# Kernel optimization log

Measured on AMD Instinct MI355X. Metric: run time of the kernel, lower is better.

The kernel has to match this reference:

```python
import jax, jax.numpy as jnp
import numpy as np

N, S, I, L, M = 4096, 8, 256, 512, 256


def setup_inputs() -> dict:
    key = jax.random.key(0)
    ks = jax.random.split(key, 13)
    sc_in = 1.0 / np.sqrt(I + L)
    sc_out = 1.0 / np.sqrt(L)
    return {
        "modulation": jax.random.normal(ks[0], (N, S * I), jnp.float32),
        "h0": jax.random.normal(ks[1], (N, S * L), jnp.float32),
        "c0": jax.random.normal(ks[2], (N, S * L), jnp.float32),
        "Wi": jax.random.normal(ks[3], (S, L, I + L), jnp.float32) * sc_in,
        "bi": jnp.full((S, L), -1.0, jnp.float32),  # init_input bias
        "Wf": jax.random.normal(ks[4], (S, L, I + L), jnp.float32) * sc_in,
        "bf": jnp.full((S, L), 1.0, jnp.float32),   # init_forget bias
        "Wg": jax.random.normal(ks[5], (S, L, I + L), jnp.float32) * sc_in,
        "bg": jnp.zeros((S, L), jnp.float32),
        "Wo": jax.random.normal(ks[6], (S, L, I + L), jnp.float32) * sc_in,
        "bo": jnp.zeros((S, L), jnp.float32),
        "Wy": jax.random.normal(ks[7], (S, M, L), jnp.float32) * sc_out,
        "by": jnp.zeros((S, M), jnp.float32),
    }


def reference(modulation, h0, c0, Wi, bi, Wf, bf, Wg, bg, Wo, bo, Wy, by):
    n = modulation.shape[0]
    x = modulation.reshape(n, S, I)          # [N,S,I]
    h = h0.reshape(n, S, L)                  # [N,S,L]
    c = c0.reshape(n, S, L)
    xh = jnp.concatenate([x, h], axis=-1)    # cat_groups: per-stream [x_s, h_s] -> [N,S,I+L]
    # grouped per-stream linear projections for the four gates
    i = jax.nn.sigmoid(jnp.einsum('nsd,sld->nsl', xh, Wi) + bi)
    f = jax.nn.sigmoid(jnp.einsum('nsd,sld->nsl', xh, Wf) + bf)
    g = jnp.tanh(jnp.einsum('nsd,sld->nsl', xh, Wg) + bg)
    o = jax.nn.sigmoid(jnp.einsum('nsd,sld->nsl', xh, Wo) + bo)
    c_new = f * c + i * g
    h_new = o * jnp.tanh(c_new)              # dropout p=0 -> identity
    y = jnp.einsum('nsl,sml->nsm', h_new, Wy) + by
    return y.reshape(n, S * M)
```

## Files before the change

### kernel.cpp

```cpp
#include <hip/hip_runtime.h>
#include <stdint.h>

#define S_ 8
#define N_ 4096
#define I_ 256
#define L_ 512
#define M_ 256
#define D_ 768

typedef __bf16 bf16x8 __attribute__((ext_vector_type(8)));
typedef float f32x4 __attribute__((ext_vector_type(4)));
typedef unsigned short ushort_t;

__device__ __forceinline__ unsigned short f2bf(float f) {
  union { float f; uint32_t u; } c; c.f = f;
  uint32_t u = c.u;
  uint32_t r = u + 0x7FFFu + ((u >> 16) & 1u);
  return (unsigned short)(r >> 16);
}

__device__ __forceinline__ float fsigmoid(float x) {
  return 1.0f / (1.0f + __expf(-x));
}
__device__ __forceinline__ float ftanh(float x) {
  float ax = fabsf(x);
  float e = __expf(-2.0f * ax);
  float t = (1.0f - e) / (1.0f + e);
  return copysignf(t, x);
}

#define GLD16(gsrc, ldst)                                                                  \
  __builtin_amdgcn_global_load_lds(                                                        \
      (const __attribute__((address_space(1))) uint32_t*)(uintptr_t)(gsrc),                \
      (__attribute__((address_space(3))) uint32_t*)(uintptr_t)(ldst), 16, 0, 0)


__global__ __launch_bounds__(256) void cast_bf16_kernel(const float* __restrict__ src,
                                                        ushort_t* __restrict__ dst, int n4) {
  int t = blockIdx.x * 256 + threadIdx.x;
  int stride = gridDim.x * 256;
  for (; t < n4; t += stride) {
    float4 v = ((const float4*)src)[t];
    ushort4 o;
    o.x = f2bf(v.x); o.y = f2bf(v.y); o.z = f2bf(v.z); o.w = f2bf(v.w);
    ((ushort4*)dst)[t] = o;
  }
}

__global__ __launch_bounds__(256) void build_xh_kernel(const float* __restrict__ mod,
                                                       const float* __restrict__ h0,
                                                       ushort_t* __restrict__ xh) {
  int t = blockIdx.x * 256 + threadIdx.x;
  const int total = S_ * N_ * (D_ / 4);
  int stride = gridDim.x * 256;
  for (; t < total; t += stride) {
    int row = t / (D_ / 4);
    int c = t - row * (D_ / 4);
    int s = row >> 12;
    int n = row & (N_ - 1);
    float4 v;
    if (c < I_ / 4)
      v = *(const float4*)(mod + (size_t)n * (S_ * I_) + s * I_ + c * 4);
    else
      v = *(const float4*)(h0 + (size_t)n * (S_ * L_) + s * L_ + (c - I_ / 4) * 4);
    ushort4 o;
    o.x = f2bf(v.x); o.y = f2bf(v.y); o.z = f2bf(v.z); o.w = f2bf(v.w);
    *(ushort4*)(xh + (size_t)t * 4) = o;
  }
}

__global__ __launch_bounds__(256, 2) void gates_kernel(
    const ushort_t* __restrict__ xh,
    const ushort_t* __restrict__ w4,
    const float* __restrict__ bi, const float* __restrict__ bff,
    const float* __restrict__ bg, const float* __restrict__ bo,
    const float* __restrict__ c0,
    ushort_t* __restrict__ hout)
{
  __shared__ __align__(16) ushort_t smem[3072 * 8];
  const int tid = threadIdx.x;
  const int lane = tid & 63;
  const int w = tid >> 6;
  const int n0 = blockIdx.x * 128;
  const int l0 = blockIdx.y * 64;
  const int s = blockIdx.z;

  f32x4 acc[4][2][4];
  #pragma unroll
  for (int g = 0; g < 4; ++g)
    #pragma unroll
    for (int rt = 0; rt < 2; ++rt)
      #pragma unroll
      for (int ct = 0; ct < 4; ++ct) {
        f32x4 z = {0.f, 0.f, 0.f, 0.f};
        acc[g][rt][ct] = z;
      }

  const size_t xh_row0 = (size_t)(s * N_ + n0) * D_;

  for (int t = 0; t < D_ / 64; ++t) {
    const int k0 = t * 64;
    #pragma unroll
    for (int it = 0; it < 4; ++it) {
      int chunk = it * 256 + tid;
      int r = chunk >> 3, c = chunk & 7;
      int cg = c ^ (r & 7);
      const ushort_t* src = xh + xh_row0 + (size_t)r * D_ + k0 + cg * 8;
      GLD16(src, &smem[(it * 256 + w * 64) * 8]);
    }
    #pragma unroll
    for (int it = 0; it < 8; ++it) {
      int chunk = it * 256 + tid;
      int g = chunk >> 9;
      int rl = (chunk >> 3) & 63;
      int c = chunk & 7;
      int cg = c ^ (rl & 7);
      const ushort_t* src = w4 + ((size_t)((g * S_ + s) * L_ + l0 + rl)) * D_ + k0 + cg * 8;
      GLD16(src, &smem[(1024 + it * 256 + w * 64) * 8]);
    }
    __syncthreads();
    #pragma unroll
    for (int kk = 0; kk < 2; ++kk) {
      const int cc = kk * 4 + (lane >> 4);
      bf16x8 a[2];
      #pragma unroll
      for (int rt = 0; rt < 2; ++rt) {
        int r = w * 32 + rt * 16 + (lane & 15);
        a[rt] = *(const bf16x8*)&smem[(r * 8 + (cc ^ (r & 7))) * 8];
      }
      #pragma unroll
      for (int g = 0; g < 4; ++g) {
        #pragma unroll
        for (int ct = 0; ct < 4; ++ct) {
          int rl = ct * 16 + (lane & 15);
          bf16x8 b = *(const bf16x8*)&smem[(1024 + (g * 64 + rl) * 8 + (cc ^ (rl & 7))) * 8];
          acc[g][0][ct] = __builtin_amdgcn_mfma_f32_16x16x32_bf16(a[0], b, acc[g][0][ct], 0, 0, 0);
          acc[g][1][ct] = __builtin_amdgcn_mfma_f32_16x16x32_bf16(a[1], b, acc[g][1][ct], 0, 0, 0);
        }
      }
    }
    __syncthreads();
  }

  #pragma unroll
  for (int ct = 0; ct < 4; ++ct) {
    const int l = l0 + ct * 16 + (lane & 15);
    const float vbi = bi[s * L_ + l];
    const float vbf = bff[s * L_ + l];
    const float vbg = bg[s * L_ + l];
    const float vbo = bo[s * L_ + l];
    #pragma unroll
    for (int rt = 0; rt < 2; ++rt) {
      #pragma unroll
      for (int j = 0; j < 4; ++j) {
        const int n = n0 + w * 32 + rt * 16 + (lane >> 4) * 4 + j;
        const float c0v = c0[(size_t)n * (S_ * L_) + s * L_ + l];
        const float iv = fsigmoid(acc[0][rt][ct][j] + vbi);
        const float fv = fsigmoid(acc[1][rt][ct][j] + vbf);
        const float gv = ftanh(acc[2][rt][ct][j] + vbg);
        const float ov = fsigmoid(acc[3][rt][ct][j] + vbo);
        const float cn = fv * c0v + iv * gv;
        const float hn = ov * ftanh(cn);
        hout[(size_t)(s * N_ + n) * L_ + l] = f2bf(hn);
      }
    }
  }
}

__global__ __launch_bounds__(256, 2) void out_kernel(
    const ushort_t* __restrict__ h,
    const ushort_t* __restrict__ wy,
    const float* __restrict__ by,
    float* __restrict__ out)
{
  __shared__ __align__(16) ushort_t smem[1536 * 8];
  const int tid = threadIdx.x;
  const int lane = tid & 63;
  const int w = tid >> 6;
  const int n0 = blockIdx.x * 128;
  const int m0 = blockIdx.y * 64;
  const int s = blockIdx.z;

  f32x4 acc[2][4];
  #pragma unroll
  for (int rt = 0; rt < 2; ++rt)
    #pragma unroll
    for (int ct = 0; ct < 4; ++ct) {
      f32x4 z = {0.f, 0.f, 0.f, 0.f};
      acc[rt][ct] = z;
    }

  const size_t h_row0 = (size_t)(s * N_ + n0) * L_;

  for (int t = 0; t < L_ / 64; ++t) {
    const int k0 = t * 64;
    #pragma unroll
    for (int it = 0; it < 4; ++it) {
      int chunk = it * 256 + tid;
      int r = chunk >> 3, c = chunk & 7;
      int cg = c ^ (r & 7);
      const ushort_t* src = h + h_row0 + (size_t)r * L_ + k0 + cg * 8;
      GLD16(src, &smem[(it * 256 + w * 64) * 8]);
    }
    #pragma unroll
    for (int it = 0; it < 2; ++it) {
      int chunk = it * 256 + tid;
      int rl = chunk >> 3, c = chunk & 7;
      int cg = c ^ (rl & 7);
      const ushort_t* src = wy + ((size_t)(s * M_ + m0 + rl)) * L_ + k0 + cg * 8;
      GLD16(src, &smem[(1024 + it * 256 + w * 64) * 8]);
    }
    __syncthreads();
    #pragma unroll
    for (int kk = 0; kk < 2; ++kk) {
      const int cc = kk * 4 + (lane >> 4);
      bf16x8 a[2];
      #pragma unroll
      for (int rt = 0; rt < 2; ++rt) {
        int r = w * 32 + rt * 16 + (lane & 15);
        a[rt] = *(const bf16x8*)&smem[(r * 8 + (cc ^ (r & 7))) * 8];
      }
      #pragma unroll
      for (int ct = 0; ct < 4; ++ct) {
        int rl = ct * 16 + (lane & 15);
        bf16x8 b = *(const bf16x8*)&smem[(1024 + rl * 8 + (cc ^ (rl & 7))) * 8];
        acc[0][ct] = __builtin_amdgcn_mfma_f32_16x16x32_bf16(a[0], b, acc[0][ct], 0, 0, 0);
        acc[1][ct] = __builtin_amdgcn_mfma_f32_16x16x32_bf16(a[1], b, acc[1][ct], 0, 0, 0);
      }
    }
    __syncthreads();
  }

  #pragma unroll
  for (int ct = 0; ct < 4; ++ct) {
    const int m = m0 + ct * 16 + (lane & 15);
    const float vb = by[s * M_ + m];
    #pragma unroll
    for (int rt = 0; rt < 2; ++rt) {
      #pragma unroll
      for (int j = 0; j < 4; ++j) {
        const int n = n0 + w * 32 + rt * 16 + (lane >> 4) * 4 + j;
        out[(size_t)n * (S_ * M_) + s * M_ + m] = acc[rt][ct][j] + vb;
      }
    }
  }
}


extern "C" void kernel_launch(void* const* d_in, const int* in_sizes, int n_in,
                              void* d_out, int out_size, void* d_ws, size_t ws_size,
                              hipStream_t stream) {
  const float* mod = (const float*)d_in[0];
  const float* h0  = (const float*)d_in[1];
  const float* c0  = (const float*)d_in[2];
  const float* Wi  = (const float*)d_in[3];
  const float* bi  = (const float*)d_in[4];
  const float* Wf  = (const float*)d_in[5];
  const float* bf  = (const float*)d_in[6];
  const float* Wg  = (const float*)d_in[7];
  const float* bg  = (const float*)d_in[8];
  const float* Wo  = (const float*)d_in[9];
  const float* bo  = (const float*)d_in[10];
  const float* Wy  = (const float*)d_in[11];
  const float* by  = (const float*)d_in[12];
  float* out = (float*)d_out;

  ushort_t* ws = (ushort_t*)d_ws;
  ushort_t* xh   = ws;
  ushort_t* w4   = xh  + (size_t)S_ * N_ * D_;
  ushort_t* wyb  = w4  + (size_t)4 * S_ * L_ * D_;
  ushort_t* hbuf = wyb + (size_t)S_ * M_ * L_;

  const int SLD4 = S_ * L_ * D_ / 4;
  cast_bf16_kernel<<<512, 256, 0, stream>>>(Wi, w4 + 0 * (size_t)S_ * L_ * D_, SLD4);
  cast_bf16_kernel<<<512, 256, 0, stream>>>(Wf, w4 + 1 * (size_t)S_ * L_ * D_, SLD4);
  cast_bf16_kernel<<<512, 256, 0, stream>>>(Wg, w4 + 2 * (size_t)S_ * L_ * D_, SLD4);
  cast_bf16_kernel<<<512, 256, 0, stream>>>(Wo, w4 + 3 * (size_t)S_ * L_ * D_, SLD4);
  cast_bf16_kernel<<<256, 256, 0, stream>>>(Wy, wyb, S_ * M_ * L_ / 4);
  build_xh_kernel<<<2048, 256, 0, stream>>>(mod, h0, xh);
  gates_kernel<<<dim3(N_ / 128, L_ / 64, S_), 256, 0, stream>>>(xh, w4, bi, bf, bg, bo, c0, hbuf);
  out_kernel<<<dim3(N_ / 128, M_ / 64, S_), 256, 0, stream>>>(hbuf, wyb, by, out);
}
```

Baseline: 227.6 us.

## Rewrite gates GEMM as 8-wave double-buffered pipelined kernel; fuse weight casts

Replaces the gates kernel with a 512-thread, 256x(4x64) tile kernel. It double-buffers A and B tiles in LDS and interleaves async global->LDS loads with MFMA phases, using explicit vmcnt/lgkmcnt waits, barriers and setprio. Blocks are remapped with an XCD-aware swizzle, and the five weight-cast launches are merged into one kernel. The goal is to hide memory latency behind compute and raise operand reuse per block, at the cost of 128KB of LDS and fragile hand-written wait counts.

Result: faster. 208.1 us (-8.6%).

```diff
diff --git a/kernel.cpp b/kernel.cpp
--- a/kernel.cpp
+++ b/kernel.cpp
@@ -7,6 +7,7 @@
 #define L_ 512
 #define M_ 256
 #define D_ 768
+#define NTg 12
 
 typedef __bf16 bf16x8 __attribute__((ext_vector_type(8)));
 typedef float f32x4 __attribute__((ext_vector_type(4)));
@@ -35,15 +36,34 @@
       (__attribute__((address_space(3))) uint32_t*)(uintptr_t)(ldst), 16, 0, 0)
 
 
-__global__ __launch_bounds__(256) void cast_bf16_kernel(const float* __restrict__ src,
-                                                        ushort_t* __restrict__ dst, int n4) {
+__global__ __launch_bounds__(256) void cast_all_kernel(
+    const float* __restrict__ Wi, const float* __restrict__ Wf,
+    const float* __restrict__ Wg, const float* __restrict__ Wo,
+    const float* __restrict__ Wy, ushort_t* __restrict__ w4,
+    ushort_t* __restrict__ wyb) {
+  const int GW = S_ * L_ * D_ / 4;
+  const int WYW = S_ * M_ * L_ / 4;
+  const int TOT = 4 * GW + WYW;
   int t = blockIdx.x * 256 + threadIdx.x;
   int stride = gridDim.x * 256;
-  for (; t < n4; t += stride) {
-    float4 v = ((const float4*)src)[t];
+  for (; t < TOT; t += stride) {
+    const float* src;
+    ushort_t* dst;
+    int off;
+    if (t < 4 * GW) {
+      int g = t / GW;
+      off = t - g * GW;
+      src = (g == 0) ? Wi : (g == 1) ? Wf : (g == 2) ? Wg : Wo;
+      dst = w4 + (size_t)g * S_ * L_ * D_;
+    } else {
+      off = t - 4 * GW;
+      src = Wy;
+      dst = wyb;
+    }
+    float4 v = ((const float4*)src)[off];
     ushort4 o;
     o.x = f2bf(v.x); o.y = f2bf(v.y); o.z = f2bf(v.z); o.w = f2bf(v.w);
-    ((ushort4*)dst)[t] = o;
+    ((ushort4*)dst)[off] = o;
   }
 }
 
@@ -69,7 +89,84 @@
   }
 }
 
-__global__ __launch_bounds__(256, 2) void gates_kernel(
+#define CA0 0
+#define CB0 2048
+#define CA1 4096
+#define CB1 6144
+
+#define STAGE_A_HALF(bufbase, half, tile) do {                                          \
+    int t_ = (tile) < NTg ? (tile) : (NTg - 1);                                         \
+    int k0_ = t_ << 6;                                                                  \
+    _Pragma("unroll")                                                                   \
+    for (int i_ = 0; i_ < 2; ++i_) {                                                    \
+      int chunk_ = i_ * 512 + tid;                                                      \
+      int r_ = chunk_ >> 3, sl_ = chunk_ & 7;                                           \
+      int rf_ = (half) * 128 + r_;                                                      \
+      const ushort_t* src_ = xh + xh_base + (size_t)rf_ * D_ + k0_ +                    \
+                             ((sl_ ^ (rf_ & 7)) << 3);                                  \
+      GLD16(src_, &smem[((bufbase) + (half) * 1024 + i_ * 512 + (w << 6)) * 8]);        \
+    }                                                                                   \
+  } while (0)
+
+#define STAGE_B_HALF(bufbase, half, tile) do {                                          \
+    int t_ = (tile) < NTg ? (tile) : (NTg - 1);                                         \
+    int k0_ = t_ << 6;                                                                  \
+    _Pragma("unroll")                                                                   \
+    for (int i_ = 0; i_ < 2; ++i_) {                                                    \
+      int chunk_ = i_ * 512 + tid;                                                      \
+      int r_ = chunk_ >> 3, sl_ = chunk_ & 7;                                           \
+      int rB_ = (half) * 128 + r_;                                                      \
+      int g_ = rB_ >> 6, ll_ = rB_ & 63;                                                \
+      const ushort_t* src_ = w4 + ((size_t)((g_ * S_ + s) * L_) + l0 + ll_) * D_ +      \
+                             k0_ + ((sl_ ^ (rB_ & 7)) << 3);                            \
+      GLD16(src_, &smem[((bufbase) + (half) * 1024 + i_ * 512 + (w << 6)) * 8]);        \
+    }                                                                                   \
+  } while (0)
+
+#define LOAD_A(kk, bufbase) do {                                                        \
+    _Pragma("unroll")                                                                   \
+    for (int rt_ = 0; rt_ < 4; ++rt_) {                                                 \
+      int r_ = (wm << 6) + (rt_ << 4) + ln15;                                           \
+      int cc_ = ((kk) << 2) + ln4;                                                      \
+      a[kk][rt_] = *(const bf16x8*)&smem[((bufbase) + r_ * 8 + (cc_ ^ (r_ & 7))) * 8];  \
+    }                                                                                   \
+  } while (0)
+
+#define LOAD_B(kk, gp, bufbase) do {                                                    \
+    _Pragma("unroll")                                                                   \
+    for (int gi_ = 0; gi_ < 2; ++gi_) {                                                 \
+      _Pragma("unroll")                                                                 \
+      for (int ct_ = 0; ct_ < 2; ++ct_) {                                               \
+        int rB_ = (((gp) * 2 + gi_) << 6) + (wl << 5) + (ct_ << 4) + ln15;              \
+        int cc_ = ((kk) << 2) + ln4;                                                    \
+        bf[gi_][ct_] = *(const bf16x8*)&smem[((bufbase) + rB_ * 8 +                     \
+                                              (cc_ ^ (rB_ & 7))) * 8];                  \
+      }                                                                                 \
+    }                                                                                   \
+  } while (0)
+
+#define DO_MFMA(kk, gp) do {                                                            \
+    _Pragma("unroll")                                                                   \
+    for (int rt_ = 0; rt_ < 4; ++rt_) {                                                 \
+      _Pragma("unroll")                                                                 \
+      for (int gi_ = 0; gi_ < 2; ++gi_) {                                               \
+        _Pragma("unroll")                                                               \
+        for (int ct_ = 0; ct_ < 2; ++ct_) {                                             \
+          int cj_ = (((gp) * 2 + gi_) << 1) + ct_;                                      \
+          acc[rt_][cj_] = __builtin_amdgcn_mfma_f32_16x16x32_bf16(                      \
+              a[kk][rt_], bf[gi_][ct_], acc[rt_][cj_], 0, 0, 0);                        \
+        }                                                                               \
+      }                                                                                 \
+    }                                                                                   \
+  } while (0)
+
+#define BAR() __builtin_amdgcn_s_barrier()
+#define LGKM0() do { asm volatile("s_waitcnt lgkmcnt(0)");                              \
+                     __builtin_amdgcn_sched_barrier(0); } while (0)
+#define VMCNT4() do { asm volatile("s_waitcnt vmcnt(4)" ::: "memory");                  \
+                      __builtin_amdgcn_sched_barrier(0); } while (0)
+
+__global__ __launch_bounds__(512, 2) void gates8_kernel(
     const ushort_t* __restrict__ xh,
     const ushort_t* __restrict__ w4,
     const float* __restrict__ bi, const float* __restrict__ bff,
@@ -77,88 +174,116 @@
     const float* __restrict__ c0,
     ushort_t* __restrict__ hout)
 {
-  __shared__ __align__(16) ushort_t smem[3072 * 8];
+  __shared__ __align__(16) ushort_t smem[65536];
   const int tid = threadIdx.x;
   const int lane = tid & 63;
+  const int ln15 = lane & 15;
+  const int ln4 = lane >> 4;
   const int w = tid >> 6;
-  const int n0 = blockIdx.x * 128;
-  const int l0 = blockIdx.y * 64;
-  const int s = blockIdx.z;
-
-  f32x4 acc[4][2][4];
+  const int wm = w >> 1;
+  const int wl = w & 1;
+
+  int bid = blockIdx.x;
+  int swz = (bid & 7) * 128 + (bid >> 3);
+  const int s = swz >> 7;
+  const int r = swz & 127;
+  const int n0 = (r >> 3) << 8;
+  const int l0 = (r & 7) << 6;
+
+  const size_t xh_base = (size_t)(s * N_ + n0) * D_;
+
+  f32x4 acc[4][8];
   #pragma unroll
-  for (int g = 0; g < 4; ++g)
-    #pragma unroll
-    for (int rt = 0; rt < 2; ++rt)
-      #pragma unroll
-      for (int ct = 0; ct < 4; ++ct) {
-        f32x4 z = {0.f, 0.f, 0.f, 0.f};
-        acc[g][rt][ct] = z;
-      }
-
-  const size_t xh_row0 = (size_t)(s * N_ + n0) * D_;
-
-  for (int t = 0; t < D_ / 64; ++t) {
-    const int k0 = t * 64;
-    #pragma unroll
-    for (int it = 0; it < 4; ++it) {
-      int chunk = it * 256 + tid;
-      int r = chunk >> 3, c = chunk & 7;
-      int cg = c ^ (r & 7);
-      const ushort_t* src = xh + xh_row0 + (size_t)r * D_ + k0 + cg * 8;
-      GLD16(src, &smem[(it * 256 + w * 64) * 8]);
-    }
-    #pragma unroll
-    for (int it = 0; it < 8; ++it) {
-      int chunk = it * 256 + tid;
-      int g = chunk >> 9;
-      int rl = (chunk >> 3) & 63;
-      int c = chunk & 7;
-      int cg = c ^ (rl & 7);
-      const ushort_t* src = w4 + ((size_t)((g * S_ + s) * L_ + l0 + rl)) * D_ + k0 + cg * 8;
-      GLD16(src, &smem[(1024 + it * 256 + w * 64) * 8]);
-    }
-    __syncthreads();
-    #pragma unroll
-    for (int kk = 0; kk < 2; ++kk) {
-      const int cc = kk * 4 + (lane >> 4);
-      bf16x8 a[2];
-      #pragma unroll
-      for (int rt = 0; rt < 2; ++rt) {
-        int r = w * 32 + rt * 16 + (lane & 15);
-        a[rt] = *(const bf16x8*)&smem[(r * 8 + (cc ^ (r & 7))) * 8];
-      }
-      #pragma unroll
-      for (int g = 0; g < 4; ++g) {
-        #pragma unroll
-        for (int ct = 0; ct < 4; ++ct) {
-          int rl = ct * 16 + (lane & 15);
-          bf16x8 b = *(const bf16x8*)&smem[(1024 + (g * 64 + rl) * 8 + (cc ^ (rl & 7))) * 8];
-          acc[g][0][ct] = __builtin_amdgcn_mfma_f32_16x16x32_bf16(a[0], b, acc[g][0][ct], 0, 0, 0);
-          acc[g][1][ct] = __builtin_amdgcn_mfma_f32_16x16x32_bf16(a[1], b, acc[g][1][ct], 0, 0, 0);
-        }
-      }
-    }
-    __syncthreads();
-  }
+  for (int i = 0; i < 4; ++i)
+    #pragma unroll
+    for (int j = 0; j < 8; ++j) {
+      f32x4 z = {0.f, 0.f, 0.f, 0.f};
+      acc[i][j] = z;
+    }
+
+  bf16x8 a[2][4];
+  bf16x8 bf[2][2];
+
+  STAGE_A_HALF(CA0, 0, 0);
+  STAGE_A_HALF(CA0, 1, 0);
+  STAGE_B_HALF(CB0, 0, 0);
+  STAGE_B_HALF(CB0, 1, 0);
+  STAGE_A_HALF(CA1, 0, 1);
+  STAGE_A_HALF(CA1, 1, 1);
+
+  for (int it = 0; it < NTg / 2; ++it) {
+    const int T = 2 * it;
+    VMCNT4();
+    STAGE_B_HALF(CB1, 0, T + 1);
+    BAR();
+    LOAD_A(0, CA0); LOAD_B(0, 0, CB0);
+    LGKM0();
+    __builtin_amdgcn_s_setprio(1); DO_MFMA(0, 0); __builtin_amdgcn_s_setprio(0);
+    BAR();
+    LOAD_A(1, CA0); LOAD_B(1, 0, CB0);
+    STAGE_B_HALF(CB1, 1, T + 1);
+    BAR();
+    LGKM0();
+    __builtin_amdgcn_s_setprio(1); DO_MFMA(1, 0); __builtin_amdgcn_s_setprio(0);
+    BAR();
+    LOAD_B(0, 1, CB0);
+    STAGE_A_HALF(CA0, 0, T + 2);
+    BAR();
+    LGKM0();
+    __builtin_amdgcn_s_setprio(1); DO_MFMA(0, 1); __builtin_amdgcn_s_setprio(0);
+    BAR();
+    LOAD_B(1, 1, CB0);
+    STAGE_A_HALF(CA0, 1, T + 2);
+    BAR();
+    LGKM0();
+    __builtin_amdgcn_s_setprio(1); DO_MFMA(1, 1); __builtin_amdgcn_s_setprio(0);
+    BAR();
+    VMCNT4();
+    STAGE_B_HALF(CB0, 0, T + 2);
+    BAR();
+    LOAD_A(0, CA1); LOAD_B(0, 0, CB1);
+    LGKM0();
+    __builtin_amdgcn_s_setprio(1); DO_MFMA(0, 0); __builtin_amdgcn_s_setprio(0);
+    BAR();
+    LOAD_A(1, CA1); LOAD_B(1, 0, CB1);
+    STAGE_B_HALF(CB0, 1, T + 2);
+    BAR();
+    LGKM0();
+    __builtin_amdgcn_s_setprio(1); DO_MFMA(1, 0); __builtin_amdgcn_s_setprio(0);
+    BAR();
+    LOAD_B(0, 1, CB1);
+    STAGE_A_HALF(CA1, 0, T + 3);
+    BAR();
+    LGKM0();
+    __builtin_amdgcn_s_setprio(1); DO_MFMA(0, 1); __builtin_amdgcn_s_setprio(0);
+    BAR();
+    LOAD_B(1, 1, CB1);
+    STAGE_A_HALF(CA1, 1, T + 3);
+    BAR();
+    LGKM0();
+    __builtin_amdgcn_s_setprio(1); DO_MFMA(1, 1); __builtin_amdgcn_s_setprio(0);
+    BAR();
+  }
+
+  asm volatile("s_waitcnt vmcnt(0)" ::: "memory");
 
   #pragma unroll
-  for (int ct = 0; ct < 4; ++ct) {
-    const int l = l0 + ct * 16 + (lane & 15);
+  for (int ct = 0; ct < 2; ++ct) {
+    const int l = l0 + (wl << 5) + (ct << 4) + ln15;
     const float vbi = bi[s * L_ + l];
     const float vbf = bff[s * L_ + l];
     const float vbg = bg[s * L_ + l];
     const float vbo = bo[s * L_ + l];
     #pragma unroll
-    for (int rt = 0; rt < 2; ++rt) {
+    for (int rt = 0; rt < 4; ++rt) {
       #pragma unroll
       for (int j = 0; j < 4; ++j) {
-        const int n = n0 + w * 32 + rt * 16 + (lane >> 4) * 4 + j;
+        const int n = n0 + (wm << 6) + (rt << 4) + (ln4 << 2) + j;
         const float c0v = c0[(size_t)n * (S_ * L_) + s * L_ + l];
-        const float iv = fsigmoid(acc[0][rt][ct][j] + vbi);
-        const float fv = fsigmoid(acc[1][rt][ct][j] + vbf);
-        const float gv = ftanh(acc[2][rt][ct][j] + vbg);
-        const float ov = fsigmoid(acc[3][rt][ct][j] + vbo);
+        const float iv = fsigmoid(acc[rt][0 + ct][j] + vbi);
+        const float fv = fsigmoid(acc[rt][2 + ct][j] + vbf);
+        const float gv = ftanh(acc[rt][4 + ct][j] + vbg);
+        const float ov = fsigmoid(acc[rt][6 + ct][j] + vbo);
         const float cn = fv * c0v + iv * gv;
         const float hn = ov * ftanh(cn);
         hout[(size_t)(s * N_ + n) * L_ + l] = f2bf(hn);
@@ -214,18 +339,18 @@
     #pragma unroll
     for (int kk = 0; kk < 2; ++kk) {
       const int cc = kk * 4 + (lane >> 4);
-      bf16x8 a[2];
+      bf16x8 av[2];
       #pragma unroll
       for (int rt = 0; rt < 2; ++rt) {
-        int r = w * 32 + rt * 16 + (lane & 15);
-        a[rt] = *(const bf16x8*)&smem[(r * 8 + (cc ^ (r & 7))) * 8];
+        int rr = w * 32 + rt * 16 + (lane & 15);
+        av[rt] = *(const bf16x8*)&smem[(rr * 8 + (cc ^ (rr & 7))) * 8];
       }
       #pragma unroll
       for (int ct = 0; ct < 4; ++ct) {
         int rl = ct * 16 + (lane & 15);
         bf16x8 b = *(const bf16x8*)&smem[(1024 + rl * 8 + (cc ^ (rl & 7))) * 8];
-        acc[0][ct] = __builtin_amdgcn_mfma_f32_16x16x32_bf16(a[0], b, acc[0][ct], 0, 0, 0);
-        acc[1][ct] = __builtin_amdgcn_mfma_f32_16x16x32_bf16(a[1], b, acc[1][ct], 0, 0, 0);
+        acc[0][ct] = __builtin_amdgcn_mfma_f32_16x16x32_bf16(av[0], b, acc[0][ct], 0, 0, 0);
+        acc[1][ct] = __builtin_amdgcn_mfma_f32_16x16x32_bf16(av[1], b, acc[1][ct], 0, 0, 0);
       }
     }
     __syncthreads();
@@ -271,13 +396,8 @@
   ushort_t* wyb  = w4  + (size_t)4 * S_ * L_ * D_;
   ushort_t* hbuf = wyb + (size_t)S_ * M_ * L_;
 
-  const int SLD4 = S_ * L_ * D_ / 4;
-  cast_bf16_kernel<<<512, 256, 0, stream>>>(Wi, w4 + 0 * (size_t)S_ * L_ * D_, SLD4);
-  cast_bf16_kernel<<<512, 256, 0, stream>>>(Wf, w4 + 1 * (size_t)S_ * L_ * D_, SLD4);
-  cast_bf16_kernel<<<512, 256, 0, stream>>>(Wg, w4 + 2 * (size_t)S_ * L_ * D_, SLD4);
-  cast_bf16_kernel<<<512, 256, 0, stream>>>(Wo, w4 + 3 * (size_t)S_ * L_ * D_, SLD4);
-  cast_bf16_kernel<<<256, 256, 0, stream>>>(Wy, wyb, S_ * M_ * L_ / 4);
+  cast_all_kernel<<<2048, 256, 0, stream>>>(Wi, Wf, Wg, Wo, Wy, w4, wyb);
   build_xh_kernel<<<2048, 256, 0, stream>>>(mod, h0, xh);
-  gates_kernel<<<dim3(N_ / 128, L_ / 64, S_), 256, 0, stream>>>(xh, w4, bi, bf, bg, bo, c0, hbuf);
+  gates8_kernel<<<1024, 512, 0, stream>>>(xh, w4, bi, bf, bg, bo, c0, hbuf);
   out_kernel<<<dim3(N_ / 128, M_ / 64, S_), 256, 0, stream>>>(hbuf, wyb, by, out);
 }
```
